# Kernel optimization log

Measured on AMD Instinct MI355X. Metric: run time of the kernel, lower is better.

The kernel has to match this reference:

```python
import jax, jax.numpy as jnp
import numpy as np

D = 768          # emb_dim (BERT hidden size)
N_DOM = 9        # domain_num
N_EXP = 6        # num_expert (per-domain)
N_SH = 4         # num_shared_expert
N_TOT = N_EXP + N_SH  # total experts seen by the gate
B = 2048


def _p(key, shape, scale=0.02):
    return jax.random.normal(key, shape, dtype=jnp.float32) * scale


def setup_inputs() -> dict:
    key = jax.random.key(0)
    ks = jax.random.split(key, 32)
    inp = {
        "content_pooled": jax.random.normal(ks[0], (B, D), dtype=jnp.float32),
        "ftr_pooled": jax.random.normal(ks[1], (B, D), dtype=jnp.float32),
        "category": jax.random.randint(ks[2], (B,), 0, N_DOM, dtype=jnp.int64),
        "domain_emb": _p(ks[3], (N_DOM, D), 1.0),
    }
    # per-domain expert stacks: Linear(D,D)-SiLU-Linear(D,D), for content (c) and ftr (f)
    for pre, base in (("c", 4), ("f", 12)):
        inp[pre + "W1"] = _p(ks[base + 0], (N_DOM, N_EXP, D, D))
        inp[pre + "b1"] = jnp.zeros((N_DOM, N_EXP, D), jnp.float32)
        inp[pre + "W2"] = _p(ks[base + 1], (N_DOM, N_EXP, D, D))
        inp[pre + "b2"] = jnp.zeros((N_DOM, N_EXP, D), jnp.float32)
        # shared experts: Linear(D,D)-SiLU-Linear(D,D)
        inp[pre + "sW1"] = _p(ks[base + 2], (N_SH, D, D))
        inp[pre + "sb1"] = jnp.zeros((N_SH, D), jnp.float32)
        inp[pre + "sW2"] = _p(ks[base + 3], (N_SH, D, D))
        inp[pre + "sb2"] = jnp.zeros((N_SH, D), jnp.float32)
        # per-domain enhanced gates: Linear(2D,D)-SiLU-Linear(D,N_TOT), temperature scalar per domain
        inp[pre + "gW1"] = _p(ks[base + 4], (N_DOM, 2 * D, D))
        inp[pre + "gb1"] = jnp.zeros((N_DOM, D), jnp.float32)
        inp[pre + "gW2"] = _p(ks[base + 5], (N_DOM, D, N_TOT))
        inp[pre + "gb2"] = jnp.zeros((N_DOM, N_TOT), jnp.float32)
        inp[pre + "temp"] = jnp.ones((N_DOM,), jnp.float32)
    return inp


def _moe_branch(x, category, domain_emb, W1, b1, W2, b2,
                sW1, sb1, sW2, sb2, gW1, gb1, gW2, gb2, temp):
    # x: [B, D]; category: [B] int in [0, N_DOM)
    demb = domain_emb[category]                           # [B, D]
    g_in = jnp.concatenate([demb, x], axis=-1)            # [B, 2D]
    # gate computed for all domains, then per-example domain selected
    gh = jax.nn.silu(jnp.einsum("bx,nxh->bnh", g_in, gW1) + gb1)      # [B, 9, D]
    logits = jnp.einsum("bnh,nhe->bne", gh, gW2) + gb2                 # [B, 9, 10]
    t = jax.nn.softplus(temp) + 1e-4                                    # positive temperature
    gates_all = jax.nn.softmax(logits / t[None, :, None], axis=-1)
    gates = jnp.take_along_axis(gates_all, category[:, None, None], axis=1)[:, 0]  # [B, 10]
    # per-domain experts for all domains (grouped GEMM form), then select domain
    h1 = jax.nn.silu(jnp.einsum("bd,nedh->bneh", x, W1) + b1)          # [B, 9, 6, D]
    e_all = jnp.einsum("bneh,nehd->bned", h1, W2) + b2                 # [B, 9, 6, D]
    e_dom = jnp.take_along_axis(e_all, category[:, None, None, None], axis=1)[:, 0]  # [B, 6, D]
    # shared experts
    hs = jax.nn.silu(jnp.einsum("bd,edh->beh", x, sW1) + sb1)          # [B, 4, D]
    e_sh = jnp.einsum("beh,ehd->bed", hs, sW2) + sb2                   # [B, 4, D]
    experts = jnp.concatenate([e_dom, e_sh], axis=1)                   # [B, 10, D]
    return jnp.einsum("be,bed->bd", gates, experts)                    # [B, D]


def reference(content_pooled, ftr_pooled, category, domain_emb,
              cW1, cb1, cW2, cb2, csW1, csb1, csW2, csb2,
              cgW1, cgb1, cgW2, cgb2, ctemp,
              fW1, fb1, fW2, fb2, fsW1, fsb1, fsW2, fsb2,
              fgW1, fgb1, fgW2, fgb2, ftemp):
    c_out = _moe_branch(content_pooled, category, domain_emb,
                        cW1, cb1, cW2, cb2, csW1, csb1, csW2, csb2,
                        cgW1, cgb1, cgW2, cgb2, ctemp)
    f_out = _moe_branch(ftr_pooled, category, domain_emb,
                        fW1, fb1, fW2, fb2, fsW1, fsb1, fsW2, fsb2,
                        fgW1, fgb1, fgW2, fgb2, ftemp)
    return jnp.concatenate([c_out, f_out], axis=-1)  # [B, 2D]
```

## Files before the change

kernel.cpp:

```cpp
#include <hip/hip_runtime.h>

#define D_ 768
#define B_ 2048
#define NDOM 9
#define NTOT 10
#define MT 128
#define NT 128
#define KT 32
#define NTILES 6
#define KI1 (D_ / KT)

#define E2   589824ull
#define E2G  1179648ull
#define OFF_WT2 31850496ull
#define OFF_SW1 63700992ull
#define OFF_SW2 66060288ull
#define OFF_GW1 68419584ull
#define ZWE     79036416ull

typedef _Float16 f16;
typedef _Float16 f16x8 __attribute__((ext_vector_type(8)));
typedef _Float16 f16x2 __attribute__((ext_vector_type(2)));
typedef float f32x4 __attribute__((ext_vector_type(4)));

typedef const __attribute__((address_space(1))) void gas_void;
typedef __attribute__((address_space(3))) void las_void;

__device__ __forceinline__ void gload16(const f16* g, f16* l) {
  __builtin_amdgcn_global_load_lds((gas_void*)g, (las_void*)l, 16, 0, 0);
}

__global__ __launch_bounds__(256) void bucket_kernel(const int* cat32, int* perm,
                                                     int* off, int* cnt, int* dom) {
  __shared__ int scnt[NDOM], soff[NDOM], scur[NDOM];
  __shared__ int odd_nz;
  int t = threadIdx.x;
  if (t == 0) odd_nz = 0;
  if (t < NDOM) scnt[t] = 0;
  __syncthreads();
  int loc = 0;
  for (int i = t; i < B_; i += 256)
    if ((i & 1) && cat32[i] != 0) loc = 1;
  if (loc) atomicOr(&odd_nz, 1);
  __syncthreads();
  int strd = odd_nz ? 1 : 2;
  for (int i = t; i < B_; i += 256) atomicAdd(&scnt[cat32[i * strd]], 1);
  __syncthreads();
  if (t == 0) { int a = 0; for (int n = 0; n < NDOM; n++) { soff[n] = a; a += scnt[n]; } }
  __syncthreads();
  if (t < NDOM) { scur[t] = soff[t]; off[t] = soff[t]; cnt[t] = scnt[t]; }
  __syncthreads();
  for (int i = t; i < B_; i += 256) {
    int n = cat32[i * strd];
    int pos = atomicAdd(&scur[n], 1);
    perm[pos] = i;
    dom[pos] = n;
  }
}

__global__ __launch_bounds__(256) void cvt_kernel(const float* src, f16* dst, int n8) {
  int i = blockIdx.x * 256 + threadIdx.x;
  if (i >= n8) return;
  const f32x4* s = (const f32x4*)(src + (size_t)i * 8);
  f32x4 a = s[0], b = s[1];
  f16x8 o;
  o[0]=(f16)a[0]; o[1]=(f16)a[1]; o[2]=(f16)a[2]; o[3]=(f16)a[3];
  o[4]=(f16)b[0]; o[5]=(f16)b[1]; o[6]=(f16)b[2]; o[7]=(f16)b[3];
  *(f16x8*)(dst + (size_t)i * 8) = o;
}

struct TRP { const float* s[10]; f16* wt; };

__global__ __launch_bounds__(256) void trans_kernel(TRP p) {
  const int m = blockIdx.z, z = m / 125, r = m % 125;
  const float* src; f16* dst; int R;
  const size_t zw = (size_t)z * ZWE;
  if (r < 54)       { src = p.s[0+z] + (size_t)r*E2;        dst = p.wt + zw + (size_t)r*E2;                 R = 768; }
  else if (r < 108) { int i=r-54;  src = p.s[2+z] + (size_t)i*E2;  dst = p.wt + zw + OFF_WT2 + (size_t)i*E2;  R = 768; }
  else if (r < 112) { int i=r-108; src = p.s[4+z] + (size_t)i*E2;  dst = p.wt + zw + OFF_SW1 + (size_t)i*E2;  R = 768; }
  else if (r < 116) { int i=r-112; src = p.s[6+z] + (size_t)i*E2;  dst = p.wt + zw + OFF_SW2 + (size_t)i*E2;  R = 768; }
  else              { int i=r-116; src = p.s[8+z] + (size_t)i*E2G; dst = p.wt + zw + OFF_GW1 + (size_t)i*E2G; R = 1536; }
  const int ty = blockIdx.y;
  if (ty * 64 >= R) return;
  const int tx = blockIdx.x;

  __shared__ f16 tile[64][72];
  const int t = threadIdx.x;
  const int lr = t >> 4, lc = (t & 15) * 4;
#pragma unroll
  for (int i = 0; i < 4; i++) {
    int row = lr + i * 16;
    f32x4 v = *(const f32x4*)(src + (size_t)(ty*64 + row) * 768 + tx*64 + lc);
    tile[lc+0][row] = (f16)v[0];
    tile[lc+1][row] = (f16)v[1];
    tile[lc+2][row] = (f16)v[2];
    tile[lc+3][row] = (f16)v[3];
  }
  __syncthreads();
  const int orow = t >> 3, oc = (t & 7) * 8;
#pragma unroll
  for (int i = 0; i < 2; i++) {
    int r2 = orow + i * 32;
    f16x8 v = *(const f16x8*)&tile[r2][oc];
    *(f16x8*)(dst + (size_t)(tx*64 + r2) * R + ty*64 + oc) = v;
  }
}

struct L1P {
  const f16* x16[2]; const f16* demb16; const f16* wt;
  const float* b1[2]; const float* sb1[2]; const float* gb1[2];
  const int* perm; const int* off; const int* cnt;
  f16* h;
};

__global__ __launch_bounds__(256, 4) void layer1_kernel(L1P p) {
  const int z = blockIdx.z;
  const int g = blockIdx.y;
  const int x = blockIdx.x;
  const int nt = x % 6;
  int mt0 = x / 6, mtstep = 4;

  int row_off, row_cnt, slot, gdom = 0, kiters = KI1;
  const f16* WT; const float* bias;
  bool isGate = false;
  const size_t zw = (size_t)z * ZWE;
  if (g < 54) {
    int n = g / 6, e = g % 6;
    row_off = p.off[n]; row_cnt = p.cnt[n];
    WT = p.wt + zw + (size_t)(n*6+e) * E2;
    bias = p.b1[z] + (n*6+e) * D_;
    slot = e;
  } else if (g < 70) {
    int s_ = g - 54, e = s_ >> 2;
    row_off = 0; row_cnt = B_;
    WT = p.wt + zw + OFF_SW1 + (size_t)e * E2;
    bias = p.sb1[z] + e * D_;
    slot = 6 + e;
    mt0 = x / 6 + 4 * (s_ & 3); mtstep = 16;
  } else {
    int n = g - 70;
    row_off = p.off[n]; row_cnt = p.cnt[n];
    WT = p.wt + zw + OFF_GW1 + (size_t)n * E2G;
    bias = p.gb1[z] + n * D_;
    slot = 10; isGate = true; gdom = n; kiters = 2 * KI1;
  }
  const int KW = isGate ? 2 * D_ : D_;

  __shared__ f16 As[2][MT][KT];
  __shared__ f16 Bs[2][MT][KT];

  const int t = threadIdx.x;
  const int wave = t >> 6, lane = t & 63;
  const int wr = (wave >> 1) * 64, wc = (wave & 1) * 64;
  const int r0 = lane & 15, q = lane >> 4;
  const int jbase = nt * NT;
  const int lrow = lane >> 2;
  const int lk = (lane & 3) * 8;

  const f16* bBase[2];
#pragma unroll
  for (int i = 0; i < 2; i++) {
    int col = jbase + 32 * wave + 16 * i + lrow;
    bBase[i] = WT + (size_t)col * KW + lk;
  }
  const f16* dB = p.demb16 + (size_t)gdom * D_ + lk;

  for (int mt = mt0; mt * MT < row_cnt; mt += mtstep) {
    const f16* aBase[2];
#pragma unroll
    for (int i = 0; i < 2; i++) {
      int rl = mt * MT + 32 * wave + 16 * i + lrow;
      int pr = p.perm[(rl < row_cnt) ? (row_off + rl) : row_off];
      aBase[i] = p.x16[z] + (size_t)pr * D_ + lk;
    }

    auto STAGE = [&](int buf, int kk) {
      const int k0 = kk * KT;
#pragma unroll
      for (int i = 0; i < 2; i++) {
        const f16* as;
        if (isGate) as = (k0 < D_) ? (dB + k0) : (aBase[i] + (k0 - D_));
        else        as = aBase[i] + k0;
        gload16(as, &As[buf][32 * wave + 16 * i][0]);
        gload16(bBase[i] + k0, &Bs[buf][32 * wave + 16 * i][0]);
      }
    };

    f32x4 acc[4][4];
#pragma unroll
    for (int a = 0; a < 4; a++)
#pragma unroll
      for (int b = 0; b < 4; b++) acc[a][b] = (f32x4){0.f, 0.f, 0.f, 0.f};

    STAGE(0, 0);
    __syncthreads();
    for (int kk = 0; kk < kiters; kk++) {
      const int cur = kk & 1;
      if (kk + 1 < kiters) STAGE(cur ^ 1, kk + 1);
      f16x8 af[4], bf[4];
#pragma unroll
      for (int m = 0; m < 4; m++) af[m] = *(const f16x8*)&As[cur][wr + m * 16 + r0][q * 8];
#pragma unroll
      for (int nn = 0; nn < 4; nn++) bf[nn] = *(const f16x8*)&Bs[cur][wc + nn * 16 + r0][q * 8];
#pragma unroll
      for (int m = 0; m < 4; m++)
#pragma unroll
        for (int nn = 0; nn < 4; nn++)
          acc[m][nn] = __builtin_amdgcn_mfma_f32_16x16x32_f16(af[m], bf[nn], acc[m][nn], 0, 0, 0);
      __syncthreads();
    }

    f16* hout = p.h + (size_t)(z * 11 + slot) * B_ * D_;
#pragma unroll
    for (int nn = 0; nn < 4; nn++) {
      const int col = jbase + wc + nn * 16 + r0;
      const float bc = bias[col];
#pragma unroll
      for (int m = 0; m < 4; m++) {
#pragma unroll
        for (int i = 0; i < 4; i++) {
          int lr = mt * MT + wr + m * 16 + q * 4 + i;
          if (lr < row_cnt) {
            float v = acc[m][nn][i] + bc;
            v = v / (1.f + __expf(-v));
            hout[(size_t)(row_off + lr) * D_ + col] = (f16)v;
          }
        }
      }
    }
  }
}

struct GP {
  const f16* h;
  const float* gW2[2]; const float* gb2[2]; const float* temp[2];
  const int* dom;
  float* gates;
};

__global__ __launch_bounds__(256) void gate_kernel(GP p) {
  int wid = (blockIdx.x * 256 + threadIdx.x) >> 6;
  int lane = threadIdx.x & 63;
  int z = wid >> 11;
  int pos = wid & (B_ - 1);
  int n = p.dom[pos];
  const f16* gh = p.h + ((size_t)(z * 11 + 10) * B_ + pos) * D_;
  const float* W = p.gW2[z] + (size_t)n * D_ * NTOT;
  float part[NTOT];
#pragma unroll
  for (int e = 0; e < NTOT; e++) part[e] = 0.f;
  for (int k = lane; k < D_; k += 64) {
    float a = (float)gh[k];
    const float* wrow = W + (size_t)k * NTOT;
#pragma unroll
    for (int e = 0; e < NTOT; e++) part[e] = fmaf(a, wrow[e], part[e]);
  }
#pragma unroll
  for (int e = 0; e < NTOT; e++) {
    float v = part[e];
#pragma unroll
    for (int s = 32; s > 0; s >>= 1) v += __shfl_xor(v, s, 64);
    part[e] = v;
  }
  float tv = p.temp[z][n];
  float tq = (tv > 15.f ? tv : log1pf(__expf(tv))) + 1e-4f;
  const float* b2 = p.gb2[z] + n * NTOT;
  float mx = -1e30f;
#pragma unroll
  for (int e = 0; e < NTOT; e++) { part[e] = (part[e] + b2[e]) / tq; mx = fmaxf(mx, part[e]); }
  float s = 0.f;
#pragma unroll
  for (int e = 0; e < NTOT; e++) { part[e] = __expf(part[e] - mx); s += part[e]; }
  float inv = 1.f / s;
  if (lane < NTOT) p.gates[((size_t)z * B_ + pos) * NTOT + lane] = part[lane] * inv;
}

struct L2P {
  const f16* h; const f16* wt;
  const float* b2[2]; const float* sb2[2];
  const float* gates;
  const int* perm; const int* off; const int* cnt;
  float* out;
};

__global__ __launch_bounds__(256, 4) void layer2_kernel(L2P p) {
  const int zz = blockIdx.z;
  const int z = zz / 5, es = zz % 5, ebase = es * 2;
  const int n = blockIdx.y;
  const int x = blockIdx.x;
  const int nt = x % 6, mt0 = x / 6;
  const int row_off = p.off[n], row_cnt = p.cnt[n];

  __shared__ f16 As[2][MT][KT];
  __shared__ f16 Bs[2][MT][KT];
  __shared__ float sg[MT][2];
  __shared__ int sperm[MT];

  const int t = threadIdx.x;
  const int wave = t >> 6, lane = t & 63;
  const int wr = (wave >> 1) * 64, wc = (wave & 1) * 64;
  const int r0 = lane & 15, q = lane >> 4;
  const int jbase = nt * NT;
  const int lrow = lane >> 2;
  const int lk = (lane & 3) * 8;

  const size_t zw = (size_t)z * ZWE;
  const f16* WB0; const f16* WB1; const float* pb[2]; size_t slotOff[2];
  {
    int e0 = ebase, e1 = ebase + 1;
    WB0 = (e0 < 6) ? (p.wt + zw + OFF_WT2 + (size_t)(n*6+e0)*E2) : (p.wt + zw + OFF_SW2 + (size_t)(e0-6)*E2);
    WB1 = (e1 < 6) ? (p.wt + zw + OFF_WT2 + (size_t)(n*6+e1)*E2) : (p.wt + zw + OFF_SW2 + (size_t)(e1-6)*E2);
    pb[0] = (e0 < 6) ? (p.b2[z] + (size_t)(n*6+e0)*D_) : (p.sb2[z] + (size_t)(e0-6)*D_);
    pb[1] = (e1 < 6) ? (p.b2[z] + (size_t)(n*6+e1)*D_) : (p.sb2[z] + (size_t)(e1-6)*D_);
    slotOff[0] = (size_t)(z*11 + e0) * B_ * D_;
    slotOff[1] = (size_t)(z*11 + e1) * B_ * D_;
  }

  const f16* bB0[2]; const f16* bB1[2];
#pragma unroll
  for (int i = 0; i < 2; i++) {
    int col = jbase + 32 * wave + 16 * i + lrow;
    bB0[i] = WB0 + (size_t)col * D_ + lk;
    bB1[i] = WB1 + (size_t)col * D_ + lk;
  }

  for (int mt = mt0; mt * MT < row_cnt; mt += 4) {
    for (int i = t; i < MT * 2; i += 256) {
      int rr = i >> 1, e = i & 1;
      int gp = row_off + mt * MT + rr;
      sg[rr][e] = (gp < B_ && (mt * MT + rr) < row_cnt)
                  ? p.gates[((size_t)z * B_ + gp) * NTOT + ebase + e] : 0.f;
    }
    for (int i = t; i < MT; i += 256) {
      int gp = row_off + mt * MT + i;
      sperm[i] = (gp < B_) ? p.perm[gp] : 0;
    }
    __syncthreads();

    const f16* aB0[2]; const f16* aB1[2];
#pragma unroll
    for (int i = 0; i < 2; i++) {
      int rl = mt * MT + 32 * wave + 16 * i + lrow;
      int rr = (rl < row_cnt) ? (row_off + rl) : row_off;
      size_t rp = (size_t)rr * D_ + lk;
      aB0[i] = p.h + slotOff[0] + rp;
      aB1[i] = p.h + slotOff[1] + rp;
    }
    f16 gA[4], gB[4];
#pragma unroll
    for (int m = 0; m < 4; m++) {
      gA[m] = (f16)sg[wr + m * 16 + r0][0];
      gB[m] = (f16)sg[wr + m * 16 + r0][1];
    }

    auto STAGE = [&](int buf, int it) {
      const int ei = (it >= KI1);
      const int k0 = (it - (ei ? KI1 : 0)) * KT;
#pragma unroll
      for (int i = 0; i < 2; i++) {
        const f16* as = (ei ? aB1[i] : aB0[i]) + k0;
        const f16* bs = (ei ? bB1[i] : bB0[i]) + k0;
        gload16(as, &As[buf][32 * wave + 16 * i][0]);
        gload16(bs, &Bs[buf][32 * wave + 16 * i][0]);
      }
    };

    f32x4 acc[4][4];
#pragma unroll
    for (int a = 0; a < 4; a++)
#pragma unroll
      for (int b = 0; b < 4; b++) acc[a][b] = (f32x4){0.f, 0.f, 0.f, 0.f};

    const int total = 2 * KI1;
    STAGE(0, 0);
    __syncthreads();
    for (int it = 0; it < total; it++) {
      const int cur = it & 1;
      if (it + 1 < total) STAGE(cur ^ 1, it + 1);
      const int ei = (it >= KI1);
      f16x8 af[4], bf[4];
#pragma unroll
      for (int m = 0; m < 4; m++) {
        af[m] = *(const f16x8*)&As[cur][wr + m * 16 + r0][q * 8];
        af[m] = af[m] * (ei ? gB[m] : gA[m]);
      }
#pragma unroll
      for (int nn = 0; nn < 4; nn++) bf[nn] = *(const f16x8*)&Bs[cur][wc + nn * 16 + r0][q * 8];
#pragma unroll
      for (int m = 0; m < 4; m++)
#pragma unroll
        for (int nn = 0; nn < 4; nn++)
          acc[m][nn] = __builtin_amdgcn_mfma_f32_16x16x32_f16(af[m], bf[nn], acc[m][nn], 0, 0, 0);
      __syncthreads();
    }

    const int zoff = z * D_;
#pragma unroll
    for (int nn = 0; nn < 4; nn++) {
      const int col = jbase + wc + nn * 16 + r0;
      float pbc0 = pb[0][col], pbc1 = pb[1][col];
#pragma unroll
      for (int m = 0; m < 4; m++) {
#pragma unroll
        for (int i = 0; i < 4; i++) {
          const int lrt = wr + m * 16 + q * 4 + i;
          if (mt * MT + lrt < row_cnt) {
            float v = acc[m][nn][i];
            v = fmaf(sg[lrt][0], pbc0, v);
            v = fmaf(sg[lrt][1], pbc1, v);
            float* dst = p.out + (size_t)sperm[lrt] * (2 * D_) + zoff + col;
            __hip_atomic_fetch_add(dst, v, __ATOMIC_RELAXED, __HIP_MEMORY_SCOPE_AGENT);
          }
        }
      }
    }
    __syncthreads();
  }
}

extern "C" void kernel_launch(void* const* d_in, const int* in_sizes, int n_in,
                              void* d_out, int out_size, void* d_ws, size_t ws_size,
                              hipStream_t stream) {
  const float* content = (const float*)d_in[0];
  const float* ftr     = (const float*)d_in[1];
  const int*   cat     = (const int*)d_in[2];
  const float* demb    = (const float*)d_in[3];

  const float* cW1  = (const float*)d_in[4];
  const float* cb1  = (const float*)d_in[5];
  const float* cW2  = (const float*)d_in[6];
  const float* cb2  = (const float*)d_in[7];
  const float* csW1 = (const float*)d_in[8];
  const float* csb1 = (const float*)d_in[9];
  const float* csW2 = (const float*)d_in[10];
  const float* csb2 = (const float*)d_in[11];
  const float* cgW1 = (const float*)d_in[12];
  const float* cgb1 = (const float*)d_in[13];
  const float* cgW2 = (const float*)d_in[14];
  const float* cgb2 = (const float*)d_in[15];
  const float* ctemp= (const float*)d_in[16];

  const float* fW1  = (const float*)d_in[17];
  const float* fb1  = (const float*)d_in[18];
  const float* fW2  = (const float*)d_in[19];
  const float* fb2  = (const float*)d_in[20];
  const float* fsW1 = (const float*)d_in[21];
  const float* fsb1 = (const float*)d_in[22];
  const float* fsW2 = (const float*)d_in[23];
  const float* fsb2 = (const float*)d_in[24];
  const float* fgW1 = (const float*)d_in[25];
  const float* fgb1 = (const float*)d_in[26];
  const float* fgW2 = (const float*)d_in[27];
  const float* fgb2 = (const float*)d_in[28];
  const float* ftemp= (const float*)d_in[29];

  char* wsb = (char*)d_ws;
  int* perm    = (int*)wsb;
  int* off     = (int*)(wsb + 8192);
  int* cnt     = (int*)(wsb + 8256);
  int* dom     = (int*)(wsb + 8320);
  float* gates = (float*)(wsb + 16512);
  f16* h       = (f16*)(wsb + 180352);
  f16* x16a    = (f16*)(wsb + 69386368);
  f16* x16b    = (f16*)(wsb + 72532096);
  f16* demb16  = (f16*)(wsb + 75677824);
  f16* wt      = (f16*)(wsb + 75691648);
  float* out   = (float*)d_out;

  (void)hipMemsetAsync(d_out, 0, (size_t)out_size * sizeof(float), stream);

  bucket_kernel<<<1, 256, 0, stream>>>(cat, perm, off, cnt, dom);

  cvt_kernel<<<768, 256, 0, stream>>>(content, x16a, (B_ * D_) / 8);
  cvt_kernel<<<768, 256, 0, stream>>>(ftr, x16b, (B_ * D_) / 8);
  cvt_kernel<<<4, 256, 0, stream>>>(demb, demb16, (NDOM * D_) / 8);

  TRP tp;
  tp.s[0] = cW1;  tp.s[1] = fW1;
  tp.s[2] = cW2;  tp.s[3] = fW2;
  tp.s[4] = csW1; tp.s[5] = fsW1;
  tp.s[6] = csW2; tp.s[7] = fsW2;
  tp.s[8] = cgW1; tp.s[9] = fgW1;
  tp.wt = wt;
  trans_kernel<<<dim3(12, 24, 250), 256, 0, stream>>>(tp);

  L1P p1;
  p1.x16[0] = x16a; p1.x16[1] = x16b; p1.demb16 = demb16; p1.wt = wt;
  p1.b1[0] = cb1;  p1.b1[1] = fb1;
  p1.sb1[0] = csb1; p1.sb1[1] = fsb1;
  p1.gb1[0] = cgb1; p1.gb1[1] = fgb1;
  p1.perm = perm; p1.off = off; p1.cnt = cnt; p1.h = h;
  layer1_kernel<<<dim3(24, 79, 2), 256, 0, stream>>>(p1);

  GP pg;
  pg.h = h; pg.gW2[0] = cgW2; pg.gW2[1] = fgW2;
  pg.gb2[0] = cgb2; pg.gb2[1] = fgb2;
  pg.temp[0] = ctemp; pg.temp[1] = ftemp;
  pg.dom = dom; pg.gates = gates;
  gate_kernel<<<dim3((2 * B_) / 4), 256, 0, stream>>>(pg);

  L2P p2;
  p2.h = h; p2.wt = wt;
  p2.b2[0] = cb2;  p2.b2[1] = fb2;
  p2.sb2[0] = csb2; p2.sb2[1] = fsb2;
  p2.gates = gates; p2.perm = perm; p2.off = off; p2.cnt = cnt; p2.out = out;
  layer2_kernel<<<dim3(24, 9, 10), 256, 0, stream>>>(p2);

  (void)in_sizes; (void)n_in; (void)ws_size;
}
```

Before: 627.1 us.

## Use triple-buffered LDS pipeline with explicit vmcnt waits in both GEMM kernels

```diff
diff --git a/kernel.cpp b/kernel.cpp
--- a/kernel.cpp
+++ b/kernel.cpp
@@ -7,7 +7,6 @@
 #define MT 128
 #define NT 128
 #define KT 32
-#define NTILES 6
 #define KI1 (D_ / KT)
 
 #define E2   589824ull
@@ -29,6 +28,10 @@
 __device__ __forceinline__ void gload16(const f16* g, f16* l) {
   __builtin_amdgcn_global_load_lds((gas_void*)g, (las_void*)l, 16, 0, 0);
 }
+
+#define WAITV4() asm volatile("s_waitcnt vmcnt(4)" ::: "memory")
+#define WAITV0() asm volatile("s_waitcnt vmcnt(0)" ::: "memory")
+#define SBAR()   do { __builtin_amdgcn_s_barrier(); __builtin_amdgcn_sched_barrier(0); } while (0)
 
 __global__ __launch_bounds__(256) void bucket_kernel(const int* cat32, int* perm,
                                                      int* off, int* cnt, int* dom) {
@@ -113,7 +116,7 @@
   f16* h;
 };
 
-__global__ __launch_bounds__(256, 4) void layer1_kernel(L1P p) {
+__global__ __launch_bounds__(256, 3) void layer1_kernel(L1P p) {
   const int z = blockIdx.z;
   const int g = blockIdx.y;
   const int x = blockIdx.x;
@@ -146,8 +149,8 @@
   }
   const int KW = isGate ? 2 * D_ : D_;
 
-  __shared__ f16 As[2][MT][KT];
-  __shared__ f16 Bs[2][MT][KT];
+  __shared__ f16 As[3][MT][KT];
+  __shared__ f16 Bs[3][MT][KT];
 
   const int t = threadIdx.x;
   const int wave = t >> 6, lane = t & 63;
@@ -193,10 +196,14 @@
       for (int b = 0; b < 4; b++) acc[a][b] = (f32x4){0.f, 0.f, 0.f, 0.f};
 
     STAGE(0, 0);
-    __syncthreads();
+    STAGE(1, 1);
+    WAITV4();
+    SBAR();
+
+    int cur = 0;
     for (int kk = 0; kk < kiters; kk++) {
-      const int cur = kk & 1;
-      if (kk + 1 < kiters) STAGE(cur ^ 1, kk + 1);
+      int pf = cur + 2; if (pf >= 3) pf -= 3;
+      if (kk + 2 < kiters) STAGE(pf, kk + 2);
       f16x8 af[4], bf[4];
 #pragma unroll
       for (int m = 0; m < 4; m++) af[m] = *(const f16x8*)&As[cur][wr + m * 16 + r0][q * 8];
@@ -207,7 +214,9 @@
 #pragma unroll
         for (int nn = 0; nn < 4; nn++)
           acc[m][nn] = __builtin_amdgcn_mfma_f32_16x16x32_f16(af[m], bf[nn], acc[m][nn], 0, 0, 0);
-      __syncthreads();
+      if (kk + 2 < kiters) { WAITV4(); } else { WAITV0(); }
+      SBAR();
+      cur = (cur == 2) ? 0 : cur + 1;
     }
 
     f16* hout = p.h + (size_t)(z * 11 + slot) * B_ * D_;
@@ -283,7 +292,7 @@
   float* out;
 };
 
-__global__ __launch_bounds__(256, 4) void layer2_kernel(L2P p) {
+__global__ __launch_bounds__(256, 3) void layer2_kernel(L2P p) {
   const int zz = blockIdx.z;
   const int z = zz / 5, es = zz % 5, ebase = es * 2;
   const int n = blockIdx.y;
@@ -291,8 +300,8 @@
   const int nt = x % 6, mt0 = x / 6;
   const int row_off = p.off[n], row_cnt = p.cnt[n];
 
-  __shared__ f16 As[2][MT][KT];
-  __shared__ f16 Bs[2][MT][KT];
+  __shared__ f16 As[3][MT][KT];
+  __shared__ f16 Bs[3][MT][KT];
   __shared__ float sg[MT][2];
   __shared__ int sperm[MT];
 
@@ -373,10 +382,14 @@
 
     const int total = 2 * KI1;
     STAGE(0, 0);
-    __syncthreads();
+    STAGE(1, 1);
+    WAITV4();
+    SBAR();
+
+    int cur = 0;
     for (int it = 0; it < total; it++) {
-      const int cur = it & 1;
-      if (it + 1 < total) STAGE(cur ^ 1, it + 1);
+      int pf = cur + 2; if (pf >= 3) pf -= 3;
+      if (it + 2 < total) STAGE(pf, it + 2);
       const int ei = (it >= KI1);
       f16x8 af[4], bf[4];
 #pragma unroll
@@ -391,7 +404,9 @@
 #pragma unroll
         for (int nn = 0; nn < 4; nn++)
           acc[m][nn] = __builtin_amdgcn_mfma_f32_16x16x32_f16(af[m], bf[nn], acc[m][nn], 0, 0, 0);
-      __syncthreads();
+      if (it + 2 < total) { WAITV4(); } else { WAITV0(); }
+      SBAR();
+      cur = (cur == 2) ? 0 : cur + 1;
     }
 
     const int zoff = z * D_;
```

New measurement: 612.5 us. 2.3% less time.

## Shrink GEMM blocks to single-wave 64x64 tiles with barrier-free pipelining and XCD remap

Applied to the files above, without the earlier changes.

```diff
diff --git a/kernel.cpp b/kernel.cpp
--- a/kernel.cpp
+++ b/kernel.cpp
@@ -4,10 +4,8 @@
 #define B_ 2048
 #define NDOM 9
 #define NTOT 10
-#define MT 128
-#define NT 128
+#define TS 64
 #define KT 32
-#define NTILES 6
 #define KI1 (D_ / KT)
 
 #define E2   589824ull
@@ -29,6 +27,11 @@
 __device__ __forceinline__ void gload16(const f16* g, f16* l) {
   __builtin_amdgcn_global_load_lds((gas_void*)g, (las_void*)l, 16, 0, 0);
 }
+
+#define WAITV8() asm volatile("s_waitcnt vmcnt(8)" ::: "memory")
+#define WAITV0() asm volatile("s_waitcnt vmcnt(0)" ::: "memory")
+#define WAITLGKM0() asm volatile("s_waitcnt lgkmcnt(0)" ::: "memory")
+#define SCHED0() __builtin_amdgcn_sched_barrier(0)
 
 __global__ __launch_bounds__(256) void bucket_kernel(const int* cat32, int* perm,
                                                      int* off, int* cnt, int* dom) {
@@ -84,25 +87,29 @@
   if (ty * 64 >= R) return;
   const int tx = blockIdx.x;
 
-  __shared__ f16 tile[64][72];
+  __shared__ float tile[64][65];
   const int t = threadIdx.x;
   const int lr = t >> 4, lc = (t & 15) * 4;
 #pragma unroll
   for (int i = 0; i < 4; i++) {
     int row = lr + i * 16;
     f32x4 v = *(const f32x4*)(src + (size_t)(ty*64 + row) * 768 + tx*64 + lc);
-    tile[lc+0][row] = (f16)v[0];
-    tile[lc+1][row] = (f16)v[1];
-    tile[lc+2][row] = (f16)v[2];
-    tile[lc+3][row] = (f16)v[3];
+    tile[lc+0][row] = v[0];
+    tile[lc+1][row] = v[1];
+    tile[lc+2][row] = v[2];
+    tile[lc+3][row] = v[3];
   }
   __syncthreads();
   const int orow = t >> 3, oc = (t & 7) * 8;
 #pragma unroll
   for (int i = 0; i < 2; i++) {
     int r2 = orow + i * 32;
-    f16x8 v = *(const f16x8*)&tile[r2][oc];
-    *(f16x8*)(dst + (size_t)(tx*64 + r2) * R + ty*64 + oc) = v;
+    f32x4 a = *(const f32x4*)&tile[r2][oc];
+    f32x4 b = *(const f32x4*)&tile[r2][oc + 4];
+    f16x8 o;
+    o[0]=(f16)a[0]; o[1]=(f16)a[1]; o[2]=(f16)a[2]; o[3]=(f16)a[3];
+    o[4]=(f16)b[0]; o[5]=(f16)b[1]; o[6]=(f16)b[2]; o[7]=(f16)b[3];
+    *(f16x8*)(dst + (size_t)(tx*64 + r2) * R + ty*64 + oc) = o;
   }
 }
 
@@ -113,12 +120,18 @@
   f16* h;
 };
 
-__global__ __launch_bounds__(256, 4) void layer1_kernel(L1P p) {
-  const int z = blockIdx.z;
-  const int g = blockIdx.y;
-  const int x = blockIdx.x;
-  const int nt = x % 6;
-  int mt0 = x / 6, mtstep = 4;
+#define NBL1 7584
+#define QX1  948
+
+__global__ __launch_bounds__(64) void layer1_kernel(L1P p) {
+  const int raw = blockIdx.x;
+  const int L = (raw & 7) * QX1 + (raw >> 3);
+  const int z = L / 3792;
+  const int rem = L - z * 3792;
+  const int g = rem / 48;
+  const int x = rem % 48;
+  const int nt = x % 12;
+  int mt0 = x / 12, mtstep = 4;
 
   int row_off, row_cnt, slot, gdom = 0, kiters = KI1;
   const f16* WT; const float* bias;
@@ -136,7 +149,7 @@
     WT = p.wt + zw + OFF_SW1 + (size_t)e * E2;
     bias = p.sb1[z] + e * D_;
     slot = 6 + e;
-    mt0 = x / 6 + 4 * (s_ & 3); mtstep = 16;
+    mt0 = x / 12 + 4 * (s_ & 3); mtstep = 16;
   } else {
     int n = g - 70;
     row_off = p.off[n]; row_cnt = p.cnt[n];
@@ -146,30 +159,29 @@
   }
   const int KW = isGate ? 2 * D_ : D_;
 
-  __shared__ f16 As[2][MT][KT];
-  __shared__ f16 Bs[2][MT][KT];
-
-  const int t = threadIdx.x;
-  const int wave = t >> 6, lane = t & 63;
-  const int wr = (wave >> 1) * 64, wc = (wave & 1) * 64;
+  __shared__ f16 As[2][TS][KT];
+  __shared__ f16 Bs[2][TS][KT];
+
+  const int lane = threadIdx.x;
   const int r0 = lane & 15, q = lane >> 4;
-  const int jbase = nt * NT;
   const int lrow = lane >> 2;
-  const int lk = (lane & 3) * 8;
-
-  const f16* bBase[2];
-#pragma unroll
-  for (int i = 0; i < 2; i++) {
-    int col = jbase + 32 * wave + 16 * i + lrow;
+  const int lk = 8 * ((lane & 3) ^ ((lane >> 3) & 3));
+  const int qa = (q ^ ((r0 >> 1) & 3)) * 8;
+  const int jbase = nt * TS;
+
+  const f16* bBase[4];
+#pragma unroll
+  for (int i = 0; i < 4; i++) {
+    int col = jbase + 16 * i + lrow;
     bBase[i] = WT + (size_t)col * KW + lk;
   }
   const f16* dB = p.demb16 + (size_t)gdom * D_ + lk;
 
-  for (int mt = mt0; mt * MT < row_cnt; mt += mtstep) {
-    const f16* aBase[2];
-#pragma unroll
-    for (int i = 0; i < 2; i++) {
-      int rl = mt * MT + 32 * wave + 16 * i + lrow;
+  for (int mt = mt0; mt * TS < row_cnt; mt += mtstep) {
+    const f16* aBase[4];
+#pragma unroll
+    for (int i = 0; i < 4; i++) {
+      int rl = mt * TS + 16 * i + lrow;
       int pr = p.perm[(rl < row_cnt) ? (row_off + rl) : row_off];
       aBase[i] = p.x16[z] + (size_t)pr * D_ + lk;
     }
@@ -177,13 +189,15 @@
     auto STAGE = [&](int buf, int kk) {
       const int k0 = kk * KT;
 #pragma unroll
-      for (int i = 0; i < 2; i++) {
+      for (int i = 0; i < 4; i++) {
         const f16* as;
         if (isGate) as = (k0 < D_) ? (dB + k0) : (aBase[i] + (k0 - D_));
         else        as = aBase[i] + k0;
-        gload16(as, &As[buf][32 * wave + 16 * i][0]);
-        gload16(bBase[i] + k0, &Bs[buf][32 * wave + 16 * i][0]);
+        gload16(as, &As[buf][16 * i][0]);
       }
+#pragma unroll
+      for (int i = 0; i < 4; i++)
+        gload16(bBase[i] + k0, &Bs[buf][16 * i][0]);
     };
 
     f32x4 acc[4][4];
@@ -193,33 +207,56 @@
       for (int b = 0; b < 4; b++) acc[a][b] = (f32x4){0.f, 0.f, 0.f, 0.f};
 
     STAGE(0, 0);
-    __syncthreads();
-    for (int kk = 0; kk < kiters; kk++) {
+    STAGE(1, 1);
+
+    for (int kk = 0; kk < kiters - 1; kk++) {
       const int cur = kk & 1;
-      if (kk + 1 < kiters) STAGE(cur ^ 1, kk + 1);
+      WAITV8();
       f16x8 af[4], bf[4];
 #pragma unroll
-      for (int m = 0; m < 4; m++) af[m] = *(const f16x8*)&As[cur][wr + m * 16 + r0][q * 8];
-#pragma unroll
-      for (int nn = 0; nn < 4; nn++) bf[nn] = *(const f16x8*)&Bs[cur][wc + nn * 16 + r0][q * 8];
+      for (int m = 0; m < 4; m++) af[m] = *(const f16x8*)&As[cur][m * 16 + r0][qa];
+#pragma unroll
+      for (int nn = 0; nn < 4; nn++) bf[nn] = *(const f16x8*)&Bs[cur][nn * 16 + r0][qa];
+      WAITLGKM0();
+      SCHED0();
+      if (kk + 2 < kiters) STAGE(cur, kk + 2);
+      __builtin_amdgcn_s_setprio(1);
 #pragma unroll
       for (int m = 0; m < 4; m++)
 #pragma unroll
         for (int nn = 0; nn < 4; nn++)
           acc[m][nn] = __builtin_amdgcn_mfma_f32_16x16x32_f16(af[m], bf[nn], acc[m][nn], 0, 0, 0);
-      __syncthreads();
+      __builtin_amdgcn_s_setprio(0);
+    }
+    {
+      const int cur = (kiters - 1) & 1;
+      WAITV0();
+      f16x8 af[4], bf[4];
+#pragma unroll
+      for (int m = 0; m < 4; m++) af[m] = *(const f16x8*)&As[cur][m * 16 + r0][qa];
+#pragma unroll
+      for (int nn = 0; nn < 4; nn++) bf[nn] = *(const f16x8*)&Bs[cur][nn * 16 + r0][qa];
+      WAITLGKM0();
+      SCHED0();
+      __builtin_amdgcn_s_setprio(1);
+#pragma unroll
+      for (int m = 0; m < 4; m++)
+#pragma unroll
+        for (int nn = 0; nn < 4; nn++)
+          acc[m][nn] = __builtin_amdgcn_mfma_f32_16x16x32_f16(af[m], bf[nn], acc[m][nn], 0, 0, 0);
+      __builtin_amdgcn_s_setprio(0);
     }
 
     f16* hout = p.h + (size_t)(z * 11 + slot) * B_ * D_;
 #pragma unroll
     for (int nn = 0; nn < 4; nn++) {
-      const int col = jbase + wc + nn * 16 + r0;
+      const int col = jbase + nn * 16 + r0;
       const float bc = bias[col];
 #pragma unroll
       for (int m = 0; m < 4; m++) {
 #pragma unroll
         for (int i = 0; i < 4; i++) {
-          int lr = mt * MT + wr + m * 16 + q * 4 + i;
+          int lr = mt * TS + m * 16 + q * 4 + i;
           if (lr < row_cnt) {
             float v = acc[m][nn][i] + bc;
             v = v / (1.f + __expf(-v));
@@ -283,26 +320,31 @@
   float* out;
 };
 
-__global__ __launch_bounds__(256, 4) void layer2_kernel(L2P p) {
-  const int zz = blockIdx.z;
+#define NBL2 4320
+#define QX2  540
+
+__global__ __launch_bounds__(64) void layer2_kernel(L2P p) {
+  const int raw = blockIdx.x;
+  const int L = (raw & 7) * QX2 + (raw >> 3);
+  const int zz = L / 432;
+  const int rem = L % 432;
+  const int n = rem / 48;
+  const int x = rem % 48;
   const int z = zz / 5, es = zz % 5, ebase = es * 2;
-  const int n = blockIdx.y;
-  const int x = blockIdx.x;
-  const int nt = x % 6, mt0 = x / 6;
+  const int nt = x % 12, mt0 = x / 12;
   const int row_off = p.off[n], row_cnt = p.cnt[n];
 
-  __shared__ f16 As[2][MT][KT];
-  __shared__ f16 Bs[2][MT][KT];
-  __shared__ float sg[MT][2];
-  __shared__ int sperm[MT];
-
-  const int t = threadIdx.x;
-  const int wave = t >> 6, lane = t & 63;
-  const int wr = (wave >> 1) * 64, wc = (wave & 1) * 64;
+  __shared__ f16 As[2][TS][KT];
+  __shared__ f16 Bs[2][TS][KT];
+  __shared__ float sg[TS][2];
+  __shared__ int sperm[TS];
+
+  const int lane = threadIdx.x;
   const int r0 = lane & 15, q = lane >> 4;
-  const int jbase = nt * NT;
   const int lrow = lane >> 2;
-  const int lk = (lane & 3) * 8;
+  const int lk = 8 * ((lane & 3) ^ ((lane >> 3) & 3));
+  const int qa = (q ^ ((r0 >> 1) & 3)) * 8;
+  const int jbase = nt * TS;
 
   const size_t zw = (size_t)z * ZWE;
   const f16* WB0; const f16* WB1; const float* pb[2]; size_t slotOff[2];
@@ -316,31 +358,27 @@
     slotOff[1] = (size_t)(z*11 + e1) * B_ * D_;
   }
 
-  const f16* bB0[2]; const f16* bB1[2];
-#pragma unroll
-  for (int i = 0; i < 2; i++) {
-    int col = jbase + 32 * wave + 16 * i + lrow;
+  const f16* bB0[4]; const f16* bB1[4];
+#pragma unroll
+  for (int i = 0; i < 4; i++) {
+    int col = jbase + 16 * i + lrow;
     bB0[i] = WB0 + (size_t)col * D_ + lk;
     bB1[i] = WB1 + (size_t)col * D_ + lk;
   }
 
-  for (int mt = mt0; mt * MT < row_cnt; mt += 4) {
-    for (int i = t; i < MT * 2; i += 256) {
-      int rr = i >> 1, e = i & 1;
-      int gp = row_off + mt * MT + rr;
-      sg[rr][e] = (gp < B_ && (mt * MT + rr) < row_cnt)
-                  ? p.gates[((size_t)z * B_ + gp) * NTOT + ebase + e] : 0.f;
-    }
-    for (int i = t; i < MT; i += 256) {
-      int gp = row_off + mt * MT + i;
-      sperm[i] = (gp < B_) ? p.perm[gp] : 0;
-    }
-    __syncthreads();
-
-    const f16* aB0[2]; const f16* aB1[2];
-#pragma unroll
-    for (int i = 0; i < 2; i++) {
-      int rl = mt * MT + 32 * wave + 16 * i + lrow;
+  for (int mt = mt0; mt * TS < row_cnt; mt += 4) {
+    {
+      int gp = row_off + mt * TS + lane;
+      bool ok = (gp < B_) && (mt * TS + lane < row_cnt);
+      sg[lane][0] = ok ? p.gates[((size_t)z * B_ + gp) * NTOT + ebase] : 0.f;
+      sg[lane][1] = ok ? p.gates[((size_t)z * B_ + gp) * NTOT + ebase + 1] : 0.f;
+      sperm[lane] = (gp < B_) ? p.perm[gp] : 0;
+    }
+
+    const f16* aB0[4]; const f16* aB1[4];
+#pragma unroll
+    for (int i = 0; i < 4; i++) {
+      int rl = mt * TS + 16 * i + lrow;
       int rr = (rl < row_cnt) ? (row_off + rl) : row_off;
       size_t rp = (size_t)rr * D_ + lk;
       aB0[i] = p.h + slotOff[0] + rp;
@@ -349,20 +387,19 @@
     f16 gA[4], gB[4];
 #pragma unroll
     for (int m = 0; m < 4; m++) {
-      gA[m] = (f16)sg[wr + m * 16 + r0][0];
-      gB[m] = (f16)sg[wr + m * 16 + r0][1];
+      gA[m] = (f16)sg[m * 16 + r0][0];
+      gB[m] = (f16)sg[m * 16 + r0][1];
     }
 
     auto STAGE = [&](int buf, int it) {
       const int ei = (it >= KI1);
       const int k0 = (it - (ei ? KI1 : 0)) * KT;
 #pragma unroll
-      for (int i = 0; i < 2; i++) {
-        const f16* as = (ei ? aB1[i] : aB0[i]) + k0;
-        const f16* bs = (ei ? bB1[i] : bB0[i]) + k0;
-        gload16(as, &As[buf][32 * wave + 16 * i][0]);
-        gload16(bs, &Bs[buf][32 * wave + 16 * i][0]);
-      }
+      for (int i = 0; i < 4; i++)
+        gload16((ei ? aB1[i] : aB0[i]) + k0, &As[buf][16 * i][0]);
+#pragma unroll
+      for (int i = 0; i < 4; i++)
+        gload16((ei ? bB1[i] : bB0[i]) + k0, &Bs[buf][16 * i][0]);
     };
 
     f32x4 acc[4][4];
@@ -373,38 +410,62 @@
 
     const int total = 2 * KI1;
     STAGE(0, 0);
-    __syncthreads();
-    for (int it = 0; it < total; it++) {
+    STAGE(1, 1);
+
+    for (int it = 0; it < total - 1; it++) {
       const int cur = it & 1;
-      if (it + 1 < total) STAGE(cur ^ 1, it + 1);
       const int ei = (it >= KI1);
+      WAITV8();
       f16x8 af[4], bf[4];
 #pragma unroll
+      for (int m = 0; m < 4; m++) af[m] = *(const f16x8*)&As[cur][m * 16 + r0][qa];
+#pragma unroll
+      for (int nn = 0; nn < 4; nn++) bf[nn] = *(const f16x8*)&Bs[cur][nn * 16 + r0][qa];
+      WAITLGKM0();
+      SCHED0();
+      if (it + 2 < total) STAGE(cur, it + 2);
+      __builtin_amdgcn_s_setprio(1);
+#pragma unroll
       for (int m = 0; m < 4; m++) {
-        af[m] = *(const f16x8*)&As[cur][wr + m * 16 + r0][q * 8];
-        af[m] = af[m] * (ei ? gB[m] : gA[m]);
+        f16x8 av = af[m] * (ei ? gB[m] : gA[m]);
+#pragma unroll
+        for (int nn = 0; nn < 4; nn++)
+          acc[m][nn] = __builtin_amdgcn_mfma_f32_16x16x32_f16(av, bf[nn], acc[m][nn], 0, 0, 0);
       }
-#pragma unroll
-      for (int nn = 0; nn < 4; nn++) bf[nn] = *(const f16x8*)&Bs[cur][wc + nn * 16 + r0][q * 8];
-#pragma unroll
-      for (int m = 0; m < 4; m++)
+      __builtin_amdgcn_s_setprio(0);
+    }
+    {
+      const int cur = (total - 1) & 1;
+      WAITV0();
+      f16x8 af[4], bf[4];
+#pragma unroll
+      for (int m = 0; m < 4; m++) af[m] = *(const f16x8*)&As[cur][m * 16 + r0][qa];
+#pragma unroll
+      for (int nn = 0; nn < 4; nn++) bf[nn] = *(const f16x8*)&Bs[cur][nn * 16 + r0][qa];
+      WAITLGKM0();
+      SCHED0();
+      __builtin_amdgcn_s_setprio(1);
+#pragma unroll
+      for (int m = 0; m < 4; m++) {
+        f16x8 av = af[m] * gB[m];
 #pragma unroll
         for (int nn = 0; nn < 4; nn++)
-          acc[m][nn] = __builtin_amdgcn_mfma_f32_16x16x32_f16(af[m], bf[nn], acc[m][nn], 0, 0, 0);
-      __syncthreads();
+          acc[m][nn] = __builtin_amdgcn_mfma_f32_16x16x32_f16(av, bf[nn], acc[m][nn], 0, 0, 0);
+      }
+      __builtin_amdgcn_s_setprio(0);
     }
 
     const int zoff = z * D_;
 #pragma unroll
     for (int nn = 0; nn < 4; nn++) {
-      const int col = jbase + wc + nn * 16 + r0;
+      const int col = jbase + nn * 16 + r0;
       float pbc0 = pb[0][col], pbc1 = pb[1][col];
 #pragma unroll
       for (int m = 0; m < 4; m++) {
 #pragma unroll
         for (int i = 0; i < 4; i++) {
-          const int lrt = wr + m * 16 + q * 4 + i;
-          if (mt * MT + lrt < row_cnt) {
+          const int lrt = m * 16 + q * 4 + i;
+          if (mt * TS + lrt < row_cnt) {
             float v = acc[m][nn][i];
             v = fmaf(sg[lrt][0], pbc0, v);
             v = fmaf(sg[lrt][1], pbc1, v);
@@ -414,7 +475,6 @@
         }
       }
     }
-    __syncthreads();
   }
 }
 
@@ -490,7 +550,7 @@
   p1.sb1[0] = csb1; p1.sb1[1] = fsb1;
   p1.gb1[0] = cgb1; p1.gb1[1] = fgb1;
   p1.perm = perm; p1.off = off; p1.cnt = cnt; p1.h = h;
-  layer1_kernel<<<dim3(24, 79, 2), 256, 0, stream>>>(p1);
+  layer1_kernel<<<dim3(NBL1), 64, 0, stream>>>(p1);
 
   GP pg;
   pg.h = h; pg.gW2[0] = cgW2; pg.gW2[1] = fgW2;
@@ -504,7 +564,7 @@
   p2.b2[0] = cb2;  p2.b2[1] = fb2;
   p2.sb2[0] = csb2; p2.sb2[1] = fsb2;
   p2.gates = gates; p2.perm = perm; p2.off = off; p2.cnt = cnt; p2.out = out;
-  layer2_kernel<<<dim3(24, 9, 10), 256, 0, stream>>>(p2);
+  layer2_kernel<<<dim3(NBL2), 64, 0, stream>>>(p2);
 
   (void)in_sizes; (void)n_in; (void)ws_size;
 }
```

New measurement: 678.4 us. 8.2% more time.

## Precompute domain gate term, pre-permute inputs, swizzle LDS, remap blocks across XCDs

Applied to the files above, without the earlier changes.

```diff
diff --git a/kernel.cpp b/kernel.cpp
--- a/kernel.cpp
+++ b/kernel.cpp
@@ -5,9 +5,7 @@
 #define NDOM 9
 #define NTOT 10
 #define MT 128
-#define NT 128
 #define KT 32
-#define NTILES 6
 #define KI1 (D_ / KT)
 
 #define E2   589824ull
@@ -20,7 +18,6 @@
 
 typedef _Float16 f16;
 typedef _Float16 f16x8 __attribute__((ext_vector_type(8)));
-typedef _Float16 f16x2 __attribute__((ext_vector_type(2)));
 typedef float f32x4 __attribute__((ext_vector_type(4)));
 
 typedef const __attribute__((address_space(1))) void gas_void;
@@ -58,15 +55,30 @@
   }
 }
 
-__global__ __launch_bounds__(256) void cvt_kernel(const float* src, f16* dst, int n8) {
+__global__ __launch_bounds__(256) void cvt_perm_kernel(const float* src, f16* dst,
+                                                       const int* perm, int n8) {
   int i = blockIdx.x * 256 + threadIdx.x;
   if (i >= n8) return;
-  const f32x4* s = (const f32x4*)(src + (size_t)i * 8);
+  int row = i / (D_ / 8), c8 = i % (D_ / 8);
+  int srow = perm[row];
+  const f32x4* s = (const f32x4*)(src + (size_t)srow * D_ + c8 * 8);
   f32x4 a = s[0], b = s[1];
   f16x8 o;
   o[0]=(f16)a[0]; o[1]=(f16)a[1]; o[2]=(f16)a[2]; o[3]=(f16)a[3];
   o[4]=(f16)b[0]; o[5]=(f16)b[1]; o[6]=(f16)b[2]; o[7]=(f16)b[3];
   *(f16x8*)(dst + (size_t)i * 8) = o;
+}
+
+struct DGP { const float* demb; const float* gW1[2]; const float* gb1[2]; float* dg; };
+
+__global__ __launch_bounds__(256) void dgate_kernel(DGP p) {
+  const int jc = blockIdx.x, n = blockIdx.y, z = blockIdx.z;
+  const int j = jc * 256 + threadIdx.x;
+  const float* W = p.gW1[z] + (size_t)n * 2 * D_ * D_;
+  const float* de = p.demb + (size_t)n * D_;
+  float acc = 0.f;
+  for (int k = 0; k < D_; k++) acc = fmaf(de[k], W[(size_t)k * D_ + j], acc);
+  p.dg[((size_t)z * NDOM + n) * D_ + j] = acc + p.gb1[z][n * D_ + j];
 }
 
 struct TRP { const float* s[10]; f16* wt; };
@@ -82,47 +94,58 @@
   else              { int i=r-116; src = p.s[8+z] + (size_t)i*E2G; dst = p.wt + zw + OFF_GW1 + (size_t)i*E2G; R = 1536; }
   const int ty = blockIdx.y;
   if (ty * 64 >= R) return;
+  if (R == 1536 && ty < 12) return;
   const int tx = blockIdx.x;
 
-  __shared__ f16 tile[64][72];
+  __shared__ float tile[64][65];
   const int t = threadIdx.x;
   const int lr = t >> 4, lc = (t & 15) * 4;
 #pragma unroll
   for (int i = 0; i < 4; i++) {
     int row = lr + i * 16;
     f32x4 v = *(const f32x4*)(src + (size_t)(ty*64 + row) * 768 + tx*64 + lc);
-    tile[lc+0][row] = (f16)v[0];
-    tile[lc+1][row] = (f16)v[1];
-    tile[lc+2][row] = (f16)v[2];
-    tile[lc+3][row] = (f16)v[3];
+    tile[lc+0][row] = v[0];
+    tile[lc+1][row] = v[1];
+    tile[lc+2][row] = v[2];
+    tile[lc+3][row] = v[3];
   }
   __syncthreads();
   const int orow = t >> 3, oc = (t & 7) * 8;
 #pragma unroll
   for (int i = 0; i < 2; i++) {
     int r2 = orow + i * 32;
-    f16x8 v = *(const f16x8*)&tile[r2][oc];
-    *(f16x8*)(dst + (size_t)(tx*64 + r2) * R + ty*64 + oc) = v;
+    f32x4 a = *(const f32x4*)&tile[r2][oc];
+    f32x4 b = *(const f32x4*)&tile[r2][oc + 4];
+    f16x8 o;
+    o[0]=(f16)a[0]; o[1]=(f16)a[1]; o[2]=(f16)a[2]; o[3]=(f16)a[3];
+    o[4]=(f16)b[0]; o[5]=(f16)b[1]; o[6]=(f16)b[2]; o[7]=(f16)b[3];
+    *(f16x8*)(dst + (size_t)(tx*64 + r2) * R + ty*64 + oc) = o;
   }
 }
 
 struct L1P {
-  const f16* x16[2]; const f16* demb16; const f16* wt;
-  const float* b1[2]; const float* sb1[2]; const float* gb1[2];
-  const int* perm; const int* off; const int* cnt;
+  const f16* x16p[2]; const f16* wt;
+  const float* b1[2]; const float* sb1[2]; const float* dg;
+  const int* off; const int* cnt;
   f16* h;
 };
 
+#define NBL1 3792
+#define QX1  474
+
 __global__ __launch_bounds__(256, 4) void layer1_kernel(L1P p) {
-  const int z = blockIdx.z;
-  const int g = blockIdx.y;
-  const int x = blockIdx.x;
+  const int raw = blockIdx.x;
+  const int L = (raw & 7) * QX1 + (raw >> 3);
+  const int z = L / 1896;
+  const int rem = L - z * 1896;
+  const int g = rem / 24;
+  const int x = rem % 24;
   const int nt = x % 6;
   int mt0 = x / 6, mtstep = 4;
 
-  int row_off, row_cnt, slot, gdom = 0, kiters = KI1;
+  int row_off, row_cnt, slot;
   const f16* WT; const float* bias;
-  bool isGate = false;
+  int KW = D_, koff = 0;
   const size_t zw = (size_t)z * ZWE;
   if (g < 54) {
     int n = g / 6, e = g % 6;
@@ -141,10 +164,10 @@
     int n = g - 70;
     row_off = p.off[n]; row_cnt = p.cnt[n];
     WT = p.wt + zw + OFF_GW1 + (size_t)n * E2G;
-    bias = p.gb1[z] + n * D_;
-    slot = 10; isGate = true; gdom = n; kiters = 2 * KI1;
-  }
-  const int KW = isGate ? 2 * D_ : D_;
+    bias = p.dg + (size_t)(z * NDOM + n) * D_;
+    slot = 10; KW = 2 * D_; koff = D_;
+  }
+  if (mt0 * MT >= row_cnt) return;
 
   __shared__ f16 As[2][MT][KT];
   __shared__ f16 Bs[2][MT][KT];
@@ -153,37 +176,34 @@
   const int wave = t >> 6, lane = t & 63;
   const int wr = (wave >> 1) * 64, wc = (wave & 1) * 64;
   const int r0 = lane & 15, q = lane >> 4;
-  const int jbase = nt * NT;
   const int lrow = lane >> 2;
-  const int lk = (lane & 3) * 8;
+  const int lk = 8 * ((lane & 3) ^ ((lane >> 3) & 3));
+  const int qa = (q ^ ((r0 >> 1) & 3)) * 8;
+  const int jbase = nt * MT;
 
   const f16* bBase[2];
 #pragma unroll
   for (int i = 0; i < 2; i++) {
     int col = jbase + 32 * wave + 16 * i + lrow;
-    bBase[i] = WT + (size_t)col * KW + lk;
-  }
-  const f16* dB = p.demb16 + (size_t)gdom * D_ + lk;
+    bBase[i] = WT + (size_t)col * KW + koff + lk;
+  }
+  const f16* xz = p.x16p[z];
 
   for (int mt = mt0; mt * MT < row_cnt; mt += mtstep) {
     const f16* aBase[2];
 #pragma unroll
     for (int i = 0; i < 2; i++) {
       int rl = mt * MT + 32 * wave + 16 * i + lrow;
-      int pr = p.perm[(rl < row_cnt) ? (row_off + rl) : row_off];
-      aBase[i] = p.x16[z] + (size_t)pr * D_ + lk;
+      if (rl >= row_cnt) rl = row_cnt - 1;
+      aBase[i] = xz + (size_t)(row_off + rl) * D_ + lk;
     }
 
     auto STAGE = [&](int buf, int kk) {
       const int k0 = kk * KT;
-#pragma unroll
-      for (int i = 0; i < 2; i++) {
-        const f16* as;
-        if (isGate) as = (k0 < D_) ? (dB + k0) : (aBase[i] + (k0 - D_));
-        else        as = aBase[i] + k0;
-        gload16(as, &As[buf][32 * wave + 16 * i][0]);
-        gload16(bBase[i] + k0, &Bs[buf][32 * wave + 16 * i][0]);
-      }
+      gload16(aBase[0] + k0, &As[buf][32 * wave][0]);
+      gload16(aBase[1] + k0, &As[buf][32 * wave + 16][0]);
+      gload16(bBase[0] + k0, &Bs[buf][32 * wave][0]);
+      gload16(bBase[1] + k0, &Bs[buf][32 * wave + 16][0]);
     };
 
     f32x4 acc[4][4];
@@ -194,14 +214,14 @@
 
     STAGE(0, 0);
     __syncthreads();
-    for (int kk = 0; kk < kiters; kk++) {
+    for (int kk = 0; kk < KI1; kk++) {
       const int cur = kk & 1;
-      if (kk + 1 < kiters) STAGE(cur ^ 1, kk + 1);
+      if (kk + 1 < KI1) STAGE(cur ^ 1, kk + 1);
       f16x8 af[4], bf[4];
 #pragma unroll
-      for (int m = 0; m < 4; m++) af[m] = *(const f16x8*)&As[cur][wr + m * 16 + r0][q * 8];
-#pragma unroll
-      for (int nn = 0; nn < 4; nn++) bf[nn] = *(const f16x8*)&Bs[cur][wc + nn * 16 + r0][q * 8];
+      for (int m = 0; m < 4; m++) af[m] = *(const f16x8*)&As[cur][wr + m * 16 + r0][qa];
+#pragma unroll
+      for (int nn = 0; nn < 4; nn++) bf[nn] = *(const f16x8*)&Bs[cur][wc + nn * 16 + r0][qa];
 #pragma unroll
       for (int m = 0; m < 4; m++)
 #pragma unroll
@@ -283,13 +303,20 @@
   float* out;
 };
 
+#define NBL2 2160
+#define QX2  270
+
 __global__ __launch_bounds__(256, 4) void layer2_kernel(L2P p) {
-  const int zz = blockIdx.z;
+  const int raw = blockIdx.x;
+  const int L = (raw & 7) * QX2 + (raw >> 3);
+  const int zz = L / 216;
+  const int rem = L % 216;
+  const int n = rem / 24;
+  const int x = rem % 24;
   const int z = zz / 5, es = zz % 5, ebase = es * 2;
-  const int n = blockIdx.y;
-  const int x = blockIdx.x;
   const int nt = x % 6, mt0 = x / 6;
   const int row_off = p.off[n], row_cnt = p.cnt[n];
+  if (mt0 * MT >= row_cnt) return;
 
   __shared__ f16 As[2][MT][KT];
   __shared__ f16 Bs[2][MT][KT];
@@ -300,9 +327,10 @@
   const int wave = t >> 6, lane = t & 63;
   const int wr = (wave >> 1) * 64, wc = (wave & 1) * 64;
   const int r0 = lane & 15, q = lane >> 4;
-  const int jbase = nt * NT;
   const int lrow = lane >> 2;
-  const int lk = (lane & 3) * 8;
+  const int lk = 8 * ((lane & 3) ^ ((lane >> 3) & 3));
+  const int qa = (q ^ ((r0 >> 1) & 3)) * 8;
+  const int jbase = nt * MT;
 
   const size_t zw = (size_t)z * ZWE;
   const f16* WB0; const f16* WB1; const float* pb[2]; size_t slotOff[2];
@@ -356,13 +384,10 @@
     auto STAGE = [&](int buf, int it) {
       const int ei = (it >= KI1);
       const int k0 = (it - (ei ? KI1 : 0)) * KT;
-#pragma unroll
-      for (int i = 0; i < 2; i++) {
-        const f16* as = (ei ? aB1[i] : aB0[i]) + k0;
-        const f16* bs = (ei ? bB1[i] : bB0[i]) + k0;
-        gload16(as, &As[buf][32 * wave + 16 * i][0]);
-        gload16(bs, &Bs[buf][32 * wave + 16 * i][0]);
-      }
+      gload16((ei ? aB1[0] : aB0[0]) + k0, &As[buf][32 * wave][0]);
+      gload16((ei ? aB1[1] : aB0[1]) + k0, &As[buf][32 * wave + 16][0]);
+      gload16((ei ? bB1[0] : bB0[0]) + k0, &Bs[buf][32 * wave][0]);
+      gload16((ei ? bB1[1] : bB0[1]) + k0, &Bs[buf][32 * wave + 16][0]);
     };
 
     f32x4 acc[4][4];
@@ -381,11 +406,11 @@
       f16x8 af[4], bf[4];
 #pragma unroll
       for (int m = 0; m < 4; m++) {
-        af[m] = *(const f16x8*)&As[cur][wr + m * 16 + r0][q * 8];
+        af[m] = *(const f16x8*)&As[cur][wr + m * 16 + r0][qa];
         af[m] = af[m] * (ei ? gB[m] : gA[m]);
       }
 #pragma unroll
-      for (int nn = 0; nn < 4; nn++) bf[nn] = *(const f16x8*)&Bs[cur][wc + nn * 16 + r0][q * 8];
+      for (int nn = 0; nn < 4; nn++) bf[nn] = *(const f16x8*)&Bs[cur][wc + nn * 16 + r0][qa];
 #pragma unroll
       for (int m = 0; m < 4; m++)
 #pragma unroll
@@ -460,10 +485,10 @@
   int* cnt     = (int*)(wsb + 8256);
   int* dom     = (int*)(wsb + 8320);
   float* gates = (float*)(wsb + 16512);
+  float* dg    = (float*)(wsb + 16512);
   f16* h       = (f16*)(wsb + 180352);
   f16* x16a    = (f16*)(wsb + 69386368);
   f16* x16b    = (f16*)(wsb + 72532096);
-  f16* demb16  = (f16*)(wsb + 75677824);
   f16* wt      = (f16*)(wsb + 75691648);
   float* out   = (float*)d_out;
 
@@ -471,9 +496,13 @@
 
   bucket_kernel<<<1, 256, 0, stream>>>(cat, perm, off, cnt, dom);
 
-  cvt_kernel<<<768, 256, 0, stream>>>(content, x16a, (B_ * D_) / 8);
-  cvt_kernel<<<768, 256, 0, stream>>>(ftr, x16b, (B_ * D_) / 8);
-  cvt_kernel<<<4, 256, 0, stream>>>(demb, demb16, (NDOM * D_) / 8);
+  cvt_perm_kernel<<<768, 256, 0, stream>>>(content, x16a, perm, (B_ * D_) / 8);
+  cvt_perm_kernel<<<768, 256, 0, stream>>>(ftr, x16b, perm, (B_ * D_) / 8);
+
+  DGP pd;
+  pd.demb = demb; pd.gW1[0] = cgW1; pd.gW1[1] = fgW1;
+  pd.gb1[0] = cgb1; pd.gb1[1] = fgb1; pd.dg = dg;
+  dgate_kernel<<<dim3(3, 9, 2), 256, 0, stream>>>(pd);
 
   TRP tp;
   tp.s[0] = cW1;  tp.s[1] = fW1;
@@ -485,12 +514,12 @@
   trans_kernel<<<dim3(12, 24, 250), 256, 0, stream>>>(tp);
 
   L1P p1;
-  p1.x16[0] = x16a; p1.x16[1] = x16b; p1.demb16 = demb16; p1.wt = wt;
+  p1.x16p[0] = x16a; p1.x16p[1] = x16b; p1.wt = wt;
   p1.b1[0] = cb1;  p1.b1[1] = fb1;
   p1.sb1[0] = csb1; p1.sb1[1] = fsb1;
-  p1.gb1[0] = cgb1; p1.gb1[1] = fgb1;
-  p1.perm = perm; p1.off = off; p1.cnt = cnt; p1.h = h;
-  layer1_kernel<<<dim3(24, 79, 2), 256, 0, stream>>>(p1);
+  p1.dg = dg;
+  p1.off = off; p1.cnt = cnt; p1.h = h;
+  layer1_kernel<<<dim3(NBL1), 256, 0, stream>>>(p1);
 
   GP pg;
   pg.h = h; pg.gW2[0] = cgW2; pg.gW2[1] = fgW2;
@@ -504,7 +533,7 @@
   p2.b2[0] = cb2;  p2.b2[1] = fb2;
   p2.sb2[0] = csb2; p2.sb2[1] = fsb2;
   p2.gates = gates; p2.perm = perm; p2.off = off; p2.cnt = cnt; p2.out = out;
-  layer2_kernel<<<dim3(24, 9, 10), 256, 0, stream>>>(p2);
+  layer2_kernel<<<dim3(NBL2), 256, 0, stream>>>(p2);
 
   (void)in_sizes; (void)n_in; (void)ws_size;
 }
```

Result: slower. 674.8 us (+7.6%).
